# Performance work log

Measured on AMD Instinct MI355X. Metric: run time of the kernel, lower is better.

The kernel has to match this reference:

```python
import jax, jax.numpy as jnp
import numpy as np

D = 1024
H = 16
B = 4
S = 2048
NEG = -1000000000.0


def setup_inputs() -> dict:
    key = jax.random.key(0)
    ks = jax.random.split(key, 12)
    s = 0.02
    inp = {
        "Q": jax.random.normal(ks[0], (B, S, D), jnp.float32),
        "K": jax.random.normal(ks[1], (B, S, D), jnp.float32),
        "V": jax.random.normal(ks[2], (B, S, D), jnp.float32),
        # causal mask, broadcastable to [B, H, S, S]
        "mask": jnp.broadcast_to(jnp.tril(jnp.ones((S, S), bool)), (B, 1, S, S)),
        "Wq": jax.random.normal(ks[3], (D, D), jnp.float32) * s,
        "bq": jnp.zeros((D,), jnp.float32),
        "Wk": jax.random.normal(ks[4], (D, D), jnp.float32) * s,
        "bk": jnp.zeros((D,), jnp.float32),
        "Wv": jax.random.normal(ks[5], (D, D), jnp.float32) * s,
        "bv": jnp.zeros((D,), jnp.float32),
        "Wo": jax.random.normal(ks[6], (D, D), jnp.float32) * s,
        "bo": jnp.zeros((D,), jnp.float32),
    }
    return inp


def reference(Q, K, V, mask, Wq, bq, Wk, bk, Wv, bv, Wo, bo):
    d = D // H  # head dim
    def split(x):  # [B,S,D] -> [B,H,S,d]
        Bx, Sx, _ = x.shape
        return x.reshape(Bx, Sx, H, d).transpose(0, 2, 1, 3)

    q = split(Q @ Wq + bq)
    k = split(K @ Wk + bk)
    v = split(V @ Wv + bv)

    scores = jnp.einsum("bhsd,bhtd->bhst", q, k) / jnp.sqrt(jnp.float32(d))
    scores = jnp.where(mask, scores, NEG)
    attn = jax.nn.softmax(scores, axis=-1)
    out = jnp.einsum("bhst,bhtd->bhsd", attn, v)  # [B,H,S,d]
    out = out.transpose(0, 2, 1, 3).reshape(Q.shape[0], Q.shape[1], D)
    return out @ Wo + bo
```

## Files before the change

kernel.cpp:

```cpp
#include <hip/hip_runtime.h>
#include <hip/hip_bf16.h>
#include <type_traits>

#define DEV __device__ __forceinline__

typedef short bf16x8 __attribute__((ext_vector_type(8)));
typedef float f32x4 __attribute__((ext_vector_type(4)));
typedef float f32x16 __attribute__((ext_vector_type(16)));
typedef unsigned u32x4 __attribute__((ext_vector_type(4)));

static DEV unsigned short f2bf(float f) {
  unsigned u = __builtin_bit_cast(unsigned, f);
  u += 0x7FFFu + ((u >> 16) & 1u);
  return (unsigned short)(u >> 16);
}

static DEV unsigned cvtpk(float lo, float hi) {
  unsigned d;
  asm("v_cvt_pk_bf16_f32 %0, %1, %2" : "=v"(d) : "v"(lo), "v"(hi));
  return d;
}

static DEV void pl32(unsigned& x, unsigned& y) {
  asm("v_permlane32_swap_b32 %0, %1" : "+v"(x), "+v"(y));
}

static DEV float vmax3(float a, float b, float c) {
  float d;
  asm("v_max3_f32 %0, %1, %2, %3" : "=v"(d) : "v"(a), "v"(b), "v"(c));
  return d;
}

static DEV void gl_lds16(const unsigned short* g, unsigned short* l) {
  __builtin_amdgcn_global_load_lds(
      (const __attribute__((address_space(1))) unsigned*)g,
      (__attribute__((address_space(3))) unsigned*)l, 16, 0, 0);
}

#define QSCALE 0.18033688f

__global__ __launch_bounds__(256) void wtrans4(const float* __restrict__ W0,
                                               const float* __restrict__ W1,
                                               const float* __restrict__ W2,
                                               const float* __restrict__ W3,
                                               unsigned short* __restrict__ T0,
                                               unsigned short* __restrict__ T1,
                                               unsigned short* __restrict__ T2,
                                               unsigned short* __restrict__ T3) {
  const int z = blockIdx.z;
  const float* W = z == 0 ? W0 : z == 1 ? W1 : z == 2 ? W2 : W3;
  unsigned short* Wt = z == 0 ? T0 : z == 1 ? T1 : z == 2 ? T2 : T3;
  const float wsc = (z == 0) ? QSCALE : 1.0f;
  __shared__ __align__(16) unsigned short T[64][72];
  const int tid = threadIdx.x;
  const int k0 = blockIdx.x * 64, n0 = blockIdx.y * 64;
  const int r = tid >> 4, c4 = (tid & 15) * 4;
  for (int j = 0; j < 4; ++j) {
    int row = j * 16 + r;
    float4 v = *(const float4*)&W[(size_t)(k0 + row) * 1024 + n0 + c4];
    ushort4 w;
    w.x = f2bf(v.x * wsc); w.y = f2bf(v.y * wsc);
    w.z = f2bf(v.z * wsc); w.w = f2bf(v.w * wsc);
    *(ushort4*)&T[row][c4] = w;
  }
  __syncthreads();
  for (int j = 0; j < 4; ++j) {
    int n = j * 16 + r;
    ushort4 w;
    w.x = T[c4 + 0][n]; w.y = T[c4 + 1][n]; w.z = T[c4 + 2][n]; w.w = T[c4 + 3][n];
    *(ushort4*)&Wt[(size_t)(n0 + n) * 1024 + k0 + c4] = w;
  }
}

__global__ __launch_bounds__(256) void xcvt3(const float* __restrict__ S0,
                                             const float* __restrict__ S1,
                                             const float* __restrict__ S2,
                                             unsigned short* __restrict__ D0,
                                             unsigned short* __restrict__ D1,
                                             unsigned short* __restrict__ D2) {
  const int z = blockIdx.z;
  const float* S = z == 0 ? S0 : z == 1 ? S1 : S2;
  unsigned short* D = z == 0 ? D0 : z == 1 ? D1 : D2;
  const size_t stride = (size_t)gridDim.x * 256 * 8;
  for (size_t i = ((size_t)blockIdx.x * 256 + threadIdx.x) * 8; i < 8u * 1024 * 1024;
       i += stride) {
    float4 a = *(const float4*)&S[i];
    float4 b = *(const float4*)&S[i + 4];
    uint4 w;
    w.x = cvtpk(a.x, a.y);
    w.y = cvtpk(a.z, a.w);
    w.z = cvtpk(b.x, b.y);
    w.w = cvtpk(b.z, b.w);
    *(uint4*)&D[i] = w;
  }
}

template <typename OutT>
DEV void gemm_lds_body(const unsigned short* __restrict__ X,
                       const unsigned short* __restrict__ Wt,
                       const float* __restrict__ bias, OutT* __restrict__ Y,
                       float bsc) {
  __shared__ __align__(16) unsigned short As[128 * 64];
  __shared__ __align__(16) unsigned short Bs[128 * 64];
  const int tid = threadIdx.x, lane = tid & 63, wid = tid >> 6;
  const int m0 = blockIdx.x * 128, n0 = blockIdx.y * 128;
  const int wm = (wid >> 1) * 64, wn = (wid & 1) * 64;
  f32x4 acc[4][4] = {};

  const int srow = wid * 32 + (lane >> 3);
  const int scol = (((lane & 7) ^ ((lane >> 3) & 7))) * 8;
  const unsigned short* gA = &X[(size_t)(m0 + srow) * 1024 + scol];
  const unsigned short* gB = &Wt[(size_t)(n0 + srow) * 1024 + scol];
  unsigned short* lA = &As[wid * 32 * 64];
  unsigned short* lB = &Bs[wid * 32 * 64];

  for (int k0 = 0; k0 < 1024; k0 += 64) {
    __syncthreads();
#pragma unroll
    for (int j = 0; j < 4; ++j) {
      gl_lds16(gA + (size_t)j * 8 * 1024 + k0, lA + j * 8 * 64);
      gl_lds16(gB + (size_t)j * 8 * 1024 + k0, lB + j * 8 * 64);
    }
    __syncthreads();
#pragma unroll
    for (int kk = 0; kk < 2; ++kk) {
      const int kb = ((kk * 4 + (lane >> 4)) ^ (lane & 7)) * 8;
      bf16x8 af[4], bfr[4];
#pragma unroll
      for (int i = 0; i < 4; ++i)
        af[i] = *(const bf16x8*)&As[(wm + i * 16 + (lane & 15)) * 64 + kb];
#pragma unroll
      for (int i = 0; i < 4; ++i)
        bfr[i] = *(const bf16x8*)&Bs[(wn + i * 16 + (lane & 15)) * 64 + kb];
      __builtin_amdgcn_s_setprio(1);
#pragma unroll
      for (int mi = 0; mi < 4; ++mi)
#pragma unroll
        for (int ni = 0; ni < 4; ++ni)
          acc[mi][ni] =
              __builtin_amdgcn_mfma_f32_16x16x32_bf16(af[mi], bfr[ni], acc[mi][ni], 0, 0, 0);
      __builtin_amdgcn_s_setprio(0);
    }
  }
  for (int ni = 0; ni < 4; ++ni) {
    const int col = n0 + wn + ni * 16 + (lane & 15);
    const float bv = bias[col] * bsc;
    for (int mi = 0; mi < 4; ++mi) {
      const int row = m0 + wm + mi * 16 + (lane >> 4) * 4;
      for (int r = 0; r < 4; ++r) {
        float v = acc[mi][ni][r] + bv;
        if constexpr (std::is_same_v<OutT, float>)
          Y[(size_t)(row + r) * 1024 + col] = v;
        else
          Y[(size_t)(row + r) * 1024 + col] = f2bf(v);
      }
    }
  }
}

__global__ __launch_bounds__(256) void gemm_qkv3(
    const unsigned short* __restrict__ X0, const unsigned short* __restrict__ X1,
    const unsigned short* __restrict__ X2, const unsigned short* __restrict__ W0,
    const unsigned short* __restrict__ W1, const unsigned short* __restrict__ W2,
    const float* __restrict__ b0, const float* __restrict__ b1,
    const float* __restrict__ b2, unsigned short* __restrict__ Y0,
    unsigned short* __restrict__ Y1, unsigned short* __restrict__ Y2) {
  const int z = blockIdx.z;
  const unsigned short* X = z == 0 ? X0 : z == 1 ? X1 : X2;
  const unsigned short* Wt = z == 0 ? W0 : z == 1 ? W1 : W2;
  const float* bias = z == 0 ? b0 : z == 1 ? b1 : b2;
  unsigned short* Y = z == 0 ? Y0 : z == 1 ? Y1 : Y2;
  gemm_lds_body<unsigned short>(X, Wt, bias, Y, z == 0 ? QSCALE : 1.0f);
}

__global__ __launch_bounds__(256) void gemm_out(const unsigned short* __restrict__ X,
                                                const unsigned short* __restrict__ Wt,
                                                const float* __restrict__ bias,
                                                float* __restrict__ Y) {
  gemm_lds_body<float>(X, Wt, bias, Y, 1.0f);
}

__global__ __launch_bounds__(256) void vtrans(const unsigned short* __restrict__ vbf,
                                              unsigned short* __restrict__ vt) {
  __shared__ __align__(16) unsigned short T[64][72];
  const int tid = threadIdx.x;
  const int s0 = blockIdx.x * 64;
  const int bh = blockIdx.y, b = bh >> 4, h = bh & 15;
  const int col0 = h * 64;
  const int rr = tid >> 3, c8 = (tid & 7) * 8;
  for (int p = 0; p < 2; ++p) {
    const int row = rr + 32 * p;
    *(uint4*)&T[row][c8] =
        *(const uint4*)&vbf[((size_t)b * 2048 + s0 + row) * 1024 + col0 + c8];
  }
  __syncthreads();
  const int dv = tid & 63, ss = (tid >> 6) * 16;
  union { uint4 v[2]; unsigned short s[16]; } o;
#pragma unroll
  for (int i = 0; i < 16; ++i) o.s[i] = T[ss + i][dv];
  *(uint4*)&vt[((size_t)bh * 64 + dv) * 2048 + s0 + ss] = o.v[0];
  *(uint4*)&vt[((size_t)bh * 64 + dv) * 2048 + s0 + ss + 8] = o.v[1];
}

__global__ __launch_bounds__(256) void attn_fwd(const unsigned short* __restrict__ Qb,
                                                const unsigned short* __restrict__ Kb,
                                                const unsigned short* __restrict__ Vt,
                                                unsigned short* __restrict__ Ob) {
  constexpr int KP = 72;
  __shared__ __align__(16) unsigned short SM[4 * 64 * KP];
  const int tid = threadIdx.x, lane = tid & 63, wid = tid >> 6;
  const int l31 = lane & 31, hi = lane >> 5;
  const int id = blockIdx.x;
  const int xcd = id & 7, idx = id >> 3;
  const int bh = xcd + 8 * (idx & 7);
  const int pairidx = idx >> 3;
  const int b = bh >> 4, h = bh & 15;
  const size_t rowbase = (size_t)b * 2048;
  const int col0 = h * 64;
  const unsigned short* Vrow = Vt + (size_t)bh * 64 * 2048;
  const int rr = tid >> 3, c8 = (tid & 7) * 8;

  for (int half = 0; half < 2; ++half) {
    const int qb = half == 0 ? pairidx : 15 - pairidx;
    const int q0 = (15 - qb) * 128;
    const int qmin = q0 + wid * 32;
    const int myq = qmin + l31;

    bf16x8 qf[4];
#pragma unroll
    for (int c = 0; c < 4; ++c)
      qf[c] = *(const bf16x8*)&Qb[(rowbase + myq) * 1024 + col0 + c * 16 + hi * 8];

    f32x16 o[2];
    o[0] = 0.f; o[1] = 0.f;
    float mrow = -1.0e30f, lrow = 0.f;

    const int ntiles = q0 / 64 + 2;
    uint4 kr0, kr1, vr0, vr1;
#define LOADT(KV0)                                                              \
  do {                                                                          \
    const int _k = (KV0);                                                       \
    kr0 = *(const uint4*)&Kb[(rowbase + _k + rr) * 1024 + col0 + c8];           \
    kr1 = *(const uint4*)&Kb[(rowbase + _k + rr + 32) * 1024 + col0 + c8];      \
    vr0 = *(const uint4*)&Vrow[(size_t)rr * 2048 + _k + c8];                    \
    vr1 = *(const uint4*)&Vrow[(size_t)(rr + 32) * 2048 + _k + c8];             \
  } while (0)

    LOADT(0);
    {
      unsigned short* Ks = SM;
      unsigned short* Vs = SM + 64 * KP;
      *(uint4*)&Ks[rr * KP + c8] = kr0;
      *(uint4*)&Ks[(rr + 32) * KP + c8] = kr1;
      *(uint4*)&Vs[rr * KP + c8] = vr0;
      *(uint4*)&Vs[(rr + 32) * KP + c8] = vr1;
      LOADT(64);
      __syncthreads();
    }

    for (int t = 0; t < ntiles; ++t) {
      const int kv0 = t * 64;
      const int p = t & 1;
      if (kv0 <= qmin + 31) {
        const unsigned short* Ks = SM + p * 128 * KP;
        const unsigned short* Vs = Ks + 64 * KP;

        f32x16 s2[2];
        s2[0] = 0.f; s2[1] = 0.f;
        __builtin_amdgcn_s_setprio(1);
#pragma unroll
        for (int m = 0; m < 2; ++m)
#pragma unroll
          for (int c = 0; c < 4; ++c) {
            bf16x8 kf = *(const bf16x8*)&Ks[(m * 32 + l31) * KP + c * 16 + hi * 8];
            s2[m] = __builtin_amdgcn_mfma_f32_32x32x16_bf16(kf, qf[c], s2[m], 0, 0, 0);
          }
        __builtin_amdgcn_s_setprio(0);

        if (kv0 + 63 > qmin) {
          const int thr = l31 + (qmin - kv0);
#pragma unroll
          for (int m = 0; m < 2; ++m)
#pragma unroll
            for (int r = 0; r < 16; ++r) {
              const int kvl = m * 32 + (r & 3) + 8 * (r >> 2) + 4 * hi;
              if (kvl > thr) s2[m][r] = -1.0e30f;
            }
        }

        float tmax = fmaxf(s2[0][0], s2[0][1]);
#pragma unroll
        for (int m = 0; m < 2; ++m)
#pragma unroll
          for (int r = m == 0 ? 2 : 0; r < 16; r += 2)
            tmax = vmax3(tmax, s2[m][r], s2[m][r + 1]);
        tmax = fmaxf(tmax, __shfl_xor(tmax, 32));
        if (__any(tmax > mrow + 11.5f)) {
          const float mnew = fmaxf(mrow, tmax);
          const float al = __builtin_amdgcn_exp2f(mrow - mnew);
          mrow = mnew;
          lrow *= al;
          o[0] *= al;
          o[1] *= al;
        }
        float rs0 = 0.f, rs1 = 0.f;
#pragma unroll
        for (int m = 0; m < 2; ++m)
#pragma unroll
          for (int r = 0; r < 16; ++r) {
            const float pz = __builtin_amdgcn_exp2f(s2[m][r] - mrow);
            s2[m][r] = pz;
            if (r & 1) rs1 += pz; else rs0 += pz;
          }
        float rs = rs0 + rs1;
        rs += __shfl_xor(rs, 32);
        lrow += rs;

        bf16x8 pf[4];
#pragma unroll
        for (int m = 0; m < 2; ++m) {
          unsigned a0 = cvtpk(s2[m][0], s2[m][1]), a1 = cvtpk(s2[m][2], s2[m][3]);
          unsigned b0 = cvtpk(s2[m][4], s2[m][5]), b1 = cvtpk(s2[m][6], s2[m][7]);
          pl32(a0, b0);
          pl32(a1, b1);
          pf[2 * m] = __builtin_bit_cast(bf16x8, (u32x4){a0, a1, b0, b1});
          unsigned c0 = cvtpk(s2[m][8], s2[m][9]), c1 = cvtpk(s2[m][10], s2[m][11]);
          unsigned d0 = cvtpk(s2[m][12], s2[m][13]), d1 = cvtpk(s2[m][14], s2[m][15]);
          pl32(c0, d0);
          pl32(c1, d1);
          pf[2 * m + 1] = __builtin_bit_cast(bf16x8, (u32x4){c0, c1, d0, d1});
        }

        __builtin_amdgcn_s_setprio(1);
#pragma unroll
        for (int nt = 0; nt < 2; ++nt)
#pragma unroll
          for (int cc = 0; cc < 4; ++cc) {
            bf16x8 vf = *(const bf16x8*)&Vs[(nt * 32 + l31) * KP + cc * 16 + hi * 8];
            o[nt] = __builtin_amdgcn_mfma_f32_32x32x16_bf16(vf, pf[cc], o[nt], 0, 0, 0);
          }
        __builtin_amdgcn_s_setprio(0);
      }
      if (t + 1 < ntiles) {
        unsigned short* Ks = SM + (p ^ 1) * 128 * KP;
        unsigned short* Vs = Ks + 64 * KP;
        *(uint4*)&Ks[rr * KP + c8] = kr0;
        *(uint4*)&Ks[(rr + 32) * KP + c8] = kr1;
        *(uint4*)&Vs[rr * KP + c8] = vr0;
        *(uint4*)&Vs[(rr + 32) * KP + c8] = vr1;
        if (t + 2 < ntiles) LOADT(kv0 + 128);
      }
      __syncthreads();
    }
#undef LOADT

    unsigned short* Os = SM + wid * 32 * KP;
    const float inv = 1.0f / lrow;
#pragma unroll
    for (int nt = 0; nt < 2; ++nt)
#pragma unroll
      for (int rq = 0; rq < 4; ++rq)
#pragma unroll
        for (int j = 0; j < 2; ++j) {
          const int r = rq * 4 + 2 * j;
          const unsigned pk = cvtpk(o[nt][r] * inv, o[nt][r + 1] * inv);
          *(unsigned*)&Os[l31 * KP + nt * 32 + 8 * rq + 4 * hi + 2 * j] = pk;
        }
    __syncthreads();
#pragma unroll
    for (int i = 0; i < 4; ++i) {
      const int qq = (lane >> 3) + i * 8;
      const int dvc = (lane & 7) * 8;
      uint4 val = *(const uint4*)&Os[qq * KP + dvc];
      *(uint4*)&Ob[(rowbase + qmin + qq) * 1024 + col0 + dvc] = val;
    }
    __syncthreads();
  }
}

extern "C" void kernel_launch(void* const* d_in, const int* in_sizes, int n_in,
                              void* d_out, int out_size, void* d_ws, size_t ws_size,
                              hipStream_t stream) {
  const float* Q  = (const float*)d_in[0];
  const float* K  = (const float*)d_in[1];
  const float* V  = (const float*)d_in[2];
  const float* Wq = (const float*)d_in[4];
  const float* bq = (const float*)d_in[5];
  const float* Wk = (const float*)d_in[6];
  const float* bk = (const float*)d_in[7];
  const float* Wv = (const float*)d_in[8];
  const float* bv = (const float*)d_in[9];
  const float* Wo = (const float*)d_in[10];
  const float* bo = (const float*)d_in[11];
  float* out = (float*)d_out;

  const size_t MB = 1024 * 1024;
  char* ws = (char*)d_ws;
  unsigned short* qb  = (unsigned short*)(ws + 0 * MB);
  unsigned short* kb  = (unsigned short*)(ws + 16 * MB);
  unsigned short* vbf = (unsigned short*)(ws + 32 * MB);
  unsigned short* vt  = (unsigned short*)(ws + 48 * MB);
  unsigned short* wtq = (unsigned short*)(ws + 64 * MB);
  unsigned short* wtk = (unsigned short*)(ws + 66 * MB);
  unsigned short* wtv = (unsigned short*)(ws + 68 * MB);
  unsigned short* wto = (unsigned short*)(ws + 70 * MB);
  unsigned short* ob  = vbf;

  wtrans4<<<dim3(16, 16, 4), 256, 0, stream>>>(Wq, Wk, Wv, Wo, wtq, wtk, wtv, wto);

  if (ws_size >= 120 * MB) {
    unsigned short* qx = (unsigned short*)(ws + 72 * MB);
    unsigned short* kx = (unsigned short*)(ws + 88 * MB);
    unsigned short* vx = (unsigned short*)(ws + 104 * MB);
    xcvt3<<<dim3(2048, 1, 3), 256, 0, stream>>>(Q, K, V, qx, kx, vx);
    gemm_qkv3<<<dim3(64, 8, 3), 256, 0, stream>>>(qx, kx, vx, wtq, wtk, wtv,
                                                  bq, bk, bv, qb, kb, vbf);
  } else {
    unsigned short* xb = vt;
    const float* Xs[3] = {Q, K, V};
    const unsigned short* Ws[3] = {wtq, wtk, wtv};
    const float* Bs[3] = {bq, bk, bv};
    unsigned short* Ys[3] = {qb, kb, vbf};
    for (int t = 0; t < 3; ++t) {
      xcvt3<<<dim3(2048, 1, 1), 256, 0, stream>>>(Xs[t], Xs[t], Xs[t], xb, xb, xb);
      gemm_qkv3<<<dim3(64, 8, 1), 256, 0, stream>>>(xb, xb, xb, Ws[t], Ws[t], Ws[t],
                                                    Bs[t], Bs[t], Bs[t],
                                                    Ys[t], Ys[t], Ys[t]);
    }
  }

  vtrans<<<dim3(32, 64), 256, 0, stream>>>(vbf, vt);

  attn_fwd<<<512, 256, 0, stream>>>(qb, kb, vt, ob);

  gemm_out<<<dim3(64, 8), 256, 0, stream>>>(ob, wto, bo, out);
}
```

Baseline: 201.1 us.

## Process both causal query blocks concurrently in 512-thread attention blocks sharing K/V tiles

The attention kernel previously looped over two query blocks (a short and a long causal range) sequentially in a 256-thread block. It now launches 512 threads, with waves 0-3 handling one query block and waves 4-7 the other, both consuming the same K/V tiles staged in shared memory. This halves the per-block K/V global traffic and LDS staging for the shared prefix and doubles waves available to hide latency. Waves of the shorter block sit idle at barriers while the longer block finishes its extra tiles, and larger blocks may reduce occupancy.

```diff
diff --git a/kernel.cpp b/kernel.cpp
--- a/kernel.cpp
+++ b/kernel.cpp
@@ -202,7 +202,7 @@
   *(uint4*)&vt[((size_t)bh * 64 + dv) * 2048 + s0 + ss + 8] = o.v[1];
 }
 
-__global__ __launch_bounds__(256) void attn_fwd(const unsigned short* __restrict__ Qb,
+__global__ __launch_bounds__(512) void attn_fwd(const unsigned short* __restrict__ Qb,
                                                 const unsigned short* __restrict__ Kb,
                                                 const unsigned short* __restrict__ Vt,
                                                 unsigned short* __restrict__ Ob) {
@@ -220,161 +220,153 @@
   const unsigned short* Vrow = Vt + (size_t)bh * 64 * 2048;
   const int rr = tid >> 3, c8 = (tid & 7) * 8;
 
-  for (int half = 0; half < 2; ++half) {
-    const int qb = half == 0 ? pairidx : 15 - pairidx;
-    const int q0 = (15 - qb) * 128;
-    const int qmin = q0 + wid * 32;
-    const int myq = qmin + l31;
-
-    bf16x8 qf[4];
-#pragma unroll
-    for (int c = 0; c < 4; ++c)
-      qf[c] = *(const bf16x8*)&Qb[(rowbase + myq) * 1024 + col0 + c * 16 + hi * 8];
-
-    f32x16 o[2];
-    o[0] = 0.f; o[1] = 0.f;
-    float mrow = -1.0e30f, lrow = 0.f;
-
-    const int ntiles = q0 / 64 + 2;
-    uint4 kr0, kr1, vr0, vr1;
-#define LOADT(KV0)                                                              \
-  do {                                                                          \
-    const int _k = (KV0);                                                       \
-    kr0 = *(const uint4*)&Kb[(rowbase + _k + rr) * 1024 + col0 + c8];           \
-    kr1 = *(const uint4*)&Kb[(rowbase + _k + rr + 32) * 1024 + col0 + c8];      \
-    vr0 = *(const uint4*)&Vrow[(size_t)rr * 2048 + _k + c8];                    \
-    vr1 = *(const uint4*)&Vrow[(size_t)(rr + 32) * 2048 + _k + c8];             \
+  const int half = wid >> 2, w4 = wid & 3;
+  const int qb = half == 0 ? pairidx : 15 - pairidx;
+  const int q0 = (15 - qb) * 128;
+  const int qmin = q0 + w4 * 32;
+  const int myq = qmin + l31;
+  const int NT = (15 - pairidx) * 2 + 2;
+
+  bf16x8 qf[4];
+#pragma unroll
+  for (int c = 0; c < 4; ++c)
+    qf[c] = *(const bf16x8*)&Qb[(rowbase + myq) * 1024 + col0 + c * 16 + hi * 8];
+
+  f32x16 o[2];
+  o[0] = 0.f; o[1] = 0.f;
+  float mrow = -1.0e30f, lrow = 0.f;
+
+  uint4 kr, vr;
+#define LOADT(KV0)                                                           \
+  do {                                                                       \
+    const int _k = (KV0);                                                    \
+    kr = *(const uint4*)&Kb[(rowbase + _k + rr) * 1024 + col0 + c8];         \
+    vr = *(const uint4*)&Vrow[(size_t)rr * 2048 + _k + c8];                  \
   } while (0)
 
-    LOADT(0);
-    {
-      unsigned short* Ks = SM;
-      unsigned short* Vs = SM + 64 * KP;
-      *(uint4*)&Ks[rr * KP + c8] = kr0;
-      *(uint4*)&Ks[(rr + 32) * KP + c8] = kr1;
-      *(uint4*)&Vs[rr * KP + c8] = vr0;
-      *(uint4*)&Vs[(rr + 32) * KP + c8] = vr1;
-      LOADT(64);
-      __syncthreads();
-    }
-
-    for (int t = 0; t < ntiles; ++t) {
-      const int kv0 = t * 64;
-      const int p = t & 1;
-      if (kv0 <= qmin + 31) {
-        const unsigned short* Ks = SM + p * 128 * KP;
-        const unsigned short* Vs = Ks + 64 * KP;
-
-        f32x16 s2[2];
-        s2[0] = 0.f; s2[1] = 0.f;
-        __builtin_amdgcn_s_setprio(1);
+  LOADT(0);
+  {
+    unsigned short* Ks = SM;
+    unsigned short* Vs = SM + 64 * KP;
+    *(uint4*)&Ks[rr * KP + c8] = kr;
+    *(uint4*)&Vs[rr * KP + c8] = vr;
+    if (NT > 1) LOADT(64);
+    __syncthreads();
+  }
+
+  for (int t = 0; t < NT; ++t) {
+    const int kv0 = t * 64;
+    const int p = t & 1;
+    if (kv0 <= qmin + 31) {
+      const unsigned short* Ks = SM + p * 128 * KP;
+      const unsigned short* Vs = Ks + 64 * KP;
+
+      f32x16 s2[2];
+      s2[0] = 0.f; s2[1] = 0.f;
+      __builtin_amdgcn_s_setprio(1);
+#pragma unroll
+      for (int m = 0; m < 2; ++m)
+#pragma unroll
+        for (int c = 0; c < 4; ++c) {
+          bf16x8 kf = *(const bf16x8*)&Ks[(m * 32 + l31) * KP + c * 16 + hi * 8];
+          s2[m] = __builtin_amdgcn_mfma_f32_32x32x16_bf16(kf, qf[c], s2[m], 0, 0, 0);
+        }
+      __builtin_amdgcn_s_setprio(0);
+
+      if (kv0 + 63 > qmin) {
+        const int thr = l31 + (qmin - kv0);
 #pragma unroll
         for (int m = 0; m < 2; ++m)
 #pragma unroll
-          for (int c = 0; c < 4; ++c) {
-            bf16x8 kf = *(const bf16x8*)&Ks[(m * 32 + l31) * KP + c * 16 + hi * 8];
-            s2[m] = __builtin_amdgcn_mfma_f32_32x32x16_bf16(kf, qf[c], s2[m], 0, 0, 0);
+          for (int r = 0; r < 16; ++r) {
+            const int kvl = m * 32 + (r & 3) + 8 * (r >> 2) + 4 * hi;
+            if (kvl > thr) s2[m][r] = -1.0e30f;
           }
-        __builtin_amdgcn_s_setprio(0);
-
-        if (kv0 + 63 > qmin) {
-          const int thr = l31 + (qmin - kv0);
-#pragma unroll
-          for (int m = 0; m < 2; ++m)
-#pragma unroll
-            for (int r = 0; r < 16; ++r) {
-              const int kvl = m * 32 + (r & 3) + 8 * (r >> 2) + 4 * hi;
-              if (kvl > thr) s2[m][r] = -1.0e30f;
-            }
+      }
+
+      float tmax = fmaxf(s2[0][0], s2[0][1]);
+#pragma unroll
+      for (int m = 0; m < 2; ++m)
+#pragma unroll
+        for (int r = m == 0 ? 2 : 0; r < 16; r += 2)
+          tmax = vmax3(tmax, s2[m][r], s2[m][r + 1]);
+      tmax = fmaxf(tmax, __shfl_xor(tmax, 32));
+      if (__any(tmax > mrow + 11.5f)) {
+        const float mnew = fmaxf(mrow, tmax);
+        const float al = __builtin_amdgcn_exp2f(mrow - mnew);
+        mrow = mnew;
+        lrow *= al;
+        o[0] *= al;
+        o[1] *= al;
+      }
+      float rs0 = 0.f, rs1 = 0.f;
+#pragma unroll
+      for (int m = 0; m < 2; ++m)
+#pragma unroll
+        for (int r = 0; r < 16; ++r) {
+          const float pz = __builtin_amdgcn_exp2f(s2[m][r] - mrow);
+          s2[m][r] = pz;
+          if (r & 1) rs1 += pz; else rs0 += pz;
         }
-
-        float tmax = fmaxf(s2[0][0], s2[0][1]);
-#pragma unroll
-        for (int m = 0; m < 2; ++m)
-#pragma unroll
-          for (int r = m == 0 ? 2 : 0; r < 16; r += 2)
-            tmax = vmax3(tmax, s2[m][r], s2[m][r + 1]);
-        tmax = fmaxf(tmax, __shfl_xor(tmax, 32));
-        if (__any(tmax > mrow + 11.5f)) {
-          const float mnew = fmaxf(mrow, tmax);
-          const float al = __builtin_amdgcn_exp2f(mrow - mnew);
-          mrow = mnew;
-          lrow *= al;
-          o[0] *= al;
-          o[1] *= al;
+      float rs = rs0 + rs1;
+      rs += __shfl_xor(rs, 32);
+      lrow += rs;
+
+      bf16x8 pf[4];
+#pragma unroll
+      for (int m = 0; m < 2; ++m) {
+        unsigned a0 = cvtpk(s2[m][0], s2[m][1]), a1 = cvtpk(s2[m][2], s2[m][3]);
+        unsigned b0 = cvtpk(s2[m][4], s2[m][5]), b1 = cvtpk(s2[m][6], s2[m][7]);
+        pl32(a0, b0);
+        pl32(a1, b1);
+        pf[2 * m] = __builtin_bit_cast(bf16x8, (u32x4){a0, a1, b0, b1});
+        unsigned c0 = cvtpk(s2[m][8], s2[m][9]), c1 = cvtpk(s2[m][10], s2[m][11]);
+        unsigned d0 = cvtpk(s2[m][12], s2[m][13]), d1 = cvtpk(s2[m][14], s2[m][15]);
+        pl32(c0, d0);
+        pl32(c1, d1);
+        pf[2 * m + 1] = __builtin_bit_cast(bf16x8, (u32x4){c0, c1, d0, d1});
+      }
+
+      __builtin_amdgcn_s_setprio(1);
+#pragma unroll
+      for (int nt = 0; nt < 2; ++nt)
+#pragma unroll
+        for (int cc = 0; cc < 4; ++cc) {
+          bf16x8 vf = *(const bf16x8*)&Vs[(nt * 32 + l31) * KP + cc * 16 + hi * 8];
+          o[nt] = __builtin_amdgcn_mfma_f32_32x32x16_bf16(vf, pf[cc], o[nt], 0, 0, 0);
         }
-        float rs0 = 0.f, rs1 = 0.f;
-#pragma unroll
-        for (int m = 0; m < 2; ++m)
-#pragma unroll
-          for (int r = 0; r < 16; ++r) {
-            const float pz = __builtin_amdgcn_exp2f(s2[m][r] - mrow);
-            s2[m][r] = pz;
-            if (r & 1) rs1 += pz; else rs0 += pz;
-          }
-        float rs = rs0 + rs1;
-        rs += __shfl_xor(rs, 32);
-        lrow += rs;
-
-        bf16x8 pf[4];
-#pragma unroll
-        for (int m = 0; m < 2; ++m) {
-          unsigned a0 = cvtpk(s2[m][0], s2[m][1]), a1 = cvtpk(s2[m][2], s2[m][3]);
-          unsigned b0 = cvtpk(s2[m][4], s2[m][5]), b1 = cvtpk(s2[m][6], s2[m][7]);
-          pl32(a0, b0);
-          pl32(a1, b1);
-          pf[2 * m] = __builtin_bit_cast(bf16x8, (u32x4){a0, a1, b0, b1});
-          unsigned c0 = cvtpk(s2[m][8], s2[m][9]), c1 = cvtpk(s2[m][10], s2[m][11]);
-          unsigned d0 = cvtpk(s2[m][12], s2[m][13]), d1 = cvtpk(s2[m][14], s2[m][15]);
-          pl32(c0, d0);
-          pl32(c1, d1);
-          pf[2 * m + 1] = __builtin_bit_cast(bf16x8, (u32x4){c0, c1, d0, d1});
-        }
-
-        __builtin_amdgcn_s_setprio(1);
-#pragma unroll
-        for (int nt = 0; nt < 2; ++nt)
-#pragma unroll
-          for (int cc = 0; cc < 4; ++cc) {
-            bf16x8 vf = *(const bf16x8*)&Vs[(nt * 32 + l31) * KP + cc * 16 + hi * 8];
-            o[nt] = __builtin_amdgcn_mfma_f32_32x32x16_bf16(vf, pf[cc], o[nt], 0, 0, 0);
-          }
-        __builtin_amdgcn_s_setprio(0);
+      __builtin_amdgcn_s_setprio(0);
+    }
+    if (t + 1 < NT) {
+      unsigned short* Ks = SM + (p ^ 1) * 128 * KP;
+      unsigned short* Vs = Ks + 64 * KP;
+      *(uint4*)&Ks[rr * KP + c8] = kr;
+      *(uint4*)&Vs[rr * KP + c8] = vr;
+      if (t + 2 < NT) LOADT(kv0 + 128);
+    }
+    __syncthreads();
+  }
+#undef LOADT
+
+  unsigned short* Os = SM + wid * 32 * KP;
+  const float inv = 1.0f / lrow;
+#pragma unroll
+  for (int nt = 0; nt < 2; ++nt)
+#pragma unroll
+    for (int rq = 0; rq < 4; ++rq)
+#pragma unroll
+      for (int j = 0; j < 2; ++j) {
+        const int r = rq * 4 + 2 * j;
+        const unsigned pk = cvtpk(o[nt][r] * inv, o[nt][r + 1] * inv);
+        *(unsigned*)&Os[l31 * KP + nt * 32 + 8 * rq + 4 * hi + 2 * j] = pk;
       }
-      if (t + 1 < ntiles) {
-        unsigned short* Ks = SM + (p ^ 1) * 128 * KP;
-        unsigned short* Vs = Ks + 64 * KP;
-        *(uint4*)&Ks[rr * KP + c8] = kr0;
-        *(uint4*)&Ks[(rr + 32) * KP + c8] = kr1;
-        *(uint4*)&Vs[rr * KP + c8] = vr0;
-        *(uint4*)&Vs[(rr + 32) * KP + c8] = vr1;
-        if (t + 2 < ntiles) LOADT(kv0 + 128);
-      }
-      __syncthreads();
-    }
-#undef LOADT
-
-    unsigned short* Os = SM + wid * 32 * KP;
-    const float inv = 1.0f / lrow;
-#pragma unroll
-    for (int nt = 0; nt < 2; ++nt)
-#pragma unroll
-      for (int rq = 0; rq < 4; ++rq)
-#pragma unroll
-        for (int j = 0; j < 2; ++j) {
-          const int r = rq * 4 + 2 * j;
-          const unsigned pk = cvtpk(o[nt][r] * inv, o[nt][r + 1] * inv);
-          *(unsigned*)&Os[l31 * KP + nt * 32 + 8 * rq + 4 * hi + 2 * j] = pk;
-        }
-    __syncthreads();
-#pragma unroll
-    for (int i = 0; i < 4; ++i) {
-      const int qq = (lane >> 3) + i * 8;
-      const int dvc = (lane & 7) * 8;
-      uint4 val = *(const uint4*)&Os[qq * KP + dvc];
-      *(uint4*)&Ob[(rowbase + qmin + qq) * 1024 + col0 + dvc] = val;
-    }
-    __syncthreads();
+  __syncthreads();
+#pragma unroll
+  for (int i = 0; i < 4; ++i) {
+    const int qq = (lane >> 3) + i * 8;
+    const int dvc = (lane & 7) * 8;
+    uint4 val = *(const uint4*)&Os[qq * KP + dvc];
+    *(uint4*)&Ob[(rowbase + qmin + qq) * 1024 + col0 + dvc] = val;
   }
 }
 
@@ -431,7 +423,7 @@
 
   vtrans<<<dim3(32, 64), 256, 0, stream>>>(vbf, vt);
 
-  attn_fwd<<<512, 256, 0, stream>>>(qb, kb, vt, ob);
+  attn_fwd<<<512, 512, 0, stream>>>(qb, kb, vt, ob);
 
   gemm_out<<<dim3(64, 8), 256, 0, stream>>>(ob, wto, bo, out);
 }
```

Measured after the change: 199.4 us. No clear change (-0.8%).

## Split paired causal q-blocks into separate workgroups and compute row sums via MFMA

Applied to the files above, without the earlier changes.

Each workgroup previously handled two query blocks (a short and a long one) to balance the causal workload. Now there is one query block per workgroup and the grid is twice as large, which adds parallelism at the cost of relying on the hardware scheduler for load balance. The softmax row-sum reduction, previously a VALU sum plus a cross-lane shuffle, is replaced by an extra MFMA against a ones vector, so the sums are taken over the bf16-rounded probabilities. This moves work from the vector ALU to the matrix units but adds four MFMAs per tile.

```diff
diff --git a/kernel.cpp b/kernel.cpp
--- a/kernel.cpp
+++ b/kernel.cpp
@@ -213,30 +213,30 @@
   const int id = blockIdx.x;
   const int xcd = id & 7, idx = id >> 3;
   const int bh = xcd + 8 * (idx & 7);
-  const int pairidx = idx >> 3;
+  const int qb = idx >> 3;
+  const int q0 = (15 - qb) * 128;
   const int b = bh >> 4, h = bh & 15;
   const size_t rowbase = (size_t)b * 2048;
   const int col0 = h * 64;
+  const int qmin = q0 + wid * 32;
+  const int myq = qmin + l31;
   const unsigned short* Vrow = Vt + (size_t)bh * 64 * 2048;
   const int rr = tid >> 3, c8 = (tid & 7) * 8;
 
-  for (int half = 0; half < 2; ++half) {
-    const int qb = half == 0 ? pairidx : 15 - pairidx;
-    const int q0 = (15 - qb) * 128;
-    const int qmin = q0 + wid * 32;
-    const int myq = qmin + l31;
-
-    bf16x8 qf[4];
-#pragma unroll
-    for (int c = 0; c < 4; ++c)
-      qf[c] = *(const bf16x8*)&Qb[(rowbase + myq) * 1024 + col0 + c * 16 + hi * 8];
-
-    f32x16 o[2];
-    o[0] = 0.f; o[1] = 0.f;
-    float mrow = -1.0e30f, lrow = 0.f;
-
-    const int ntiles = q0 / 64 + 2;
-    uint4 kr0, kr1, vr0, vr1;
+  bf16x8 qf[4];
+#pragma unroll
+  for (int c = 0; c < 4; ++c)
+    qf[c] = *(const bf16x8*)&Qb[(rowbase + myq) * 1024 + col0 + c * 16 + hi * 8];
+
+  const bf16x8 onesv =
+      __builtin_bit_cast(bf16x8, (u32x4){0x3F803F80u, 0x3F803F80u, 0x3F803F80u, 0x3F803F80u});
+
+  f32x16 o[2], rsa;
+  o[0] = 0.f; o[1] = 0.f; rsa = 0.f;
+  float mrow = -1.0e30f;
+
+  const int NT = q0 / 64 + 2;
+  uint4 kr0, kr1, vr0, vr1;
 #define LOADT(KV0)                                                              \
   do {                                                                          \
     const int _k = (KV0);                                                       \
@@ -246,135 +246,129 @@
     vr1 = *(const uint4*)&Vrow[(size_t)(rr + 32) * 2048 + _k + c8];             \
   } while (0)
 
-    LOADT(0);
-    {
-      unsigned short* Ks = SM;
-      unsigned short* Vs = SM + 64 * KP;
+  LOADT(0);
+  {
+    unsigned short* Ks = SM;
+    unsigned short* Vs = SM + 64 * KP;
+    *(uint4*)&Ks[rr * KP + c8] = kr0;
+    *(uint4*)&Ks[(rr + 32) * KP + c8] = kr1;
+    *(uint4*)&Vs[rr * KP + c8] = vr0;
+    *(uint4*)&Vs[(rr + 32) * KP + c8] = vr1;
+    LOADT(64);
+    __syncthreads();
+  }
+
+  for (int t = 0; t < NT; ++t) {
+    const int kv0 = t * 64;
+    const int p = t & 1;
+    if (kv0 <= qmin + 31) {
+      const unsigned short* Ks = SM + p * 128 * KP;
+      const unsigned short* Vs = Ks + 64 * KP;
+
+      f32x16 s2[2];
+      s2[0] = 0.f; s2[1] = 0.f;
+      __builtin_amdgcn_s_setprio(1);
+#pragma unroll
+      for (int m = 0; m < 2; ++m)
+#pragma unroll
+        for (int c = 0; c < 4; ++c) {
+          bf16x8 kf = *(const bf16x8*)&Ks[(m * 32 + l31) * KP + c * 16 + hi * 8];
+          s2[m] = __builtin_amdgcn_mfma_f32_32x32x16_bf16(kf, qf[c], s2[m], 0, 0, 0);
+        }
+      __builtin_amdgcn_s_setprio(0);
+
+      if (kv0 + 63 > qmin) {
+        const int thr = l31 + (qmin - kv0);
+#pragma unroll
+        for (int m = 0; m < 2; ++m)
+#pragma unroll
+          for (int r = 0; r < 16; ++r) {
+            const int kvl = m * 32 + (r & 3) + 8 * (r >> 2) + 4 * hi;
+            if (kvl > thr) s2[m][r] = -1.0e30f;
+          }
+      }
+
+      float tmax = fmaxf(s2[0][0], s2[0][1]);
+#pragma unroll
+      for (int m = 0; m < 2; ++m)
+#pragma unroll
+        for (int r = m == 0 ? 2 : 0; r < 16; r += 2)
+          tmax = vmax3(tmax, s2[m][r], s2[m][r + 1]);
+      tmax = fmaxf(tmax, __shfl_xor(tmax, 32));
+      if (__any(tmax > mrow + 11.5f)) {
+        const float mnew = fmaxf(mrow, tmax);
+        const float al = __builtin_amdgcn_exp2f(mrow - mnew);
+        mrow = mnew;
+        o[0] *= al;
+        o[1] *= al;
+        rsa[0] *= al;
+      }
+#pragma unroll
+      for (int m = 0; m < 2; ++m)
+#pragma unroll
+        for (int r = 0; r < 16; ++r)
+          s2[m][r] = __builtin_amdgcn_exp2f(s2[m][r] - mrow);
+
+      bf16x8 pf[4];
+#pragma unroll
+      for (int m = 0; m < 2; ++m) {
+        unsigned a0 = cvtpk(s2[m][0], s2[m][1]), a1 = cvtpk(s2[m][2], s2[m][3]);
+        unsigned b0 = cvtpk(s2[m][4], s2[m][5]), b1 = cvtpk(s2[m][6], s2[m][7]);
+        pl32(a0, b0);
+        pl32(a1, b1);
+        pf[2 * m] = __builtin_bit_cast(bf16x8, (u32x4){a0, a1, b0, b1});
+        unsigned c0 = cvtpk(s2[m][8], s2[m][9]), c1 = cvtpk(s2[m][10], s2[m][11]);
+        unsigned d0 = cvtpk(s2[m][12], s2[m][13]), d1 = cvtpk(s2[m][14], s2[m][15]);
+        pl32(c0, d0);
+        pl32(c1, d1);
+        pf[2 * m + 1] = __builtin_bit_cast(bf16x8, (u32x4){c0, c1, d0, d1});
+      }
+
+      __builtin_amdgcn_s_setprio(1);
+#pragma unroll
+      for (int nt = 0; nt < 2; ++nt)
+#pragma unroll
+        for (int cc = 0; cc < 4; ++cc) {
+          bf16x8 vf = *(const bf16x8*)&Vs[(nt * 32 + l31) * KP + cc * 16 + hi * 8];
+          o[nt] = __builtin_amdgcn_mfma_f32_32x32x16_bf16(vf, pf[cc], o[nt], 0, 0, 0);
+        }
+#pragma unroll
+      for (int cc = 0; cc < 4; ++cc)
+        rsa = __builtin_amdgcn_mfma_f32_32x32x16_bf16(onesv, pf[cc], rsa, 0, 0, 0);
+      __builtin_amdgcn_s_setprio(0);
+    }
+    if (t + 1 < NT) {
+      unsigned short* Ks = SM + (p ^ 1) * 128 * KP;
+      unsigned short* Vs = Ks + 64 * KP;
       *(uint4*)&Ks[rr * KP + c8] = kr0;
       *(uint4*)&Ks[(rr + 32) * KP + c8] = kr1;
       *(uint4*)&Vs[rr * KP + c8] = vr0;
       *(uint4*)&Vs[(rr + 32) * KP + c8] = vr1;
-      LOADT(64);
-      __syncthreads();
-    }
-
-    for (int t = 0; t < ntiles; ++t) {
-      const int kv0 = t * 64;
-      const int p = t & 1;
-      if (kv0 <= qmin + 31) {
-        const unsigned short* Ks = SM + p * 128 * KP;
-        const unsigned short* Vs = Ks + 64 * KP;
-
-        f32x16 s2[2];
-        s2[0] = 0.f; s2[1] = 0.f;
-        __builtin_amdgcn_s_setprio(1);
-#pragma unroll
-        for (int m = 0; m < 2; ++m)
-#pragma unroll
-          for (int c = 0; c < 4; ++c) {
-            bf16x8 kf = *(const bf16x8*)&Ks[(m * 32 + l31) * KP + c * 16 + hi * 8];
-            s2[m] = __builtin_amdgcn_mfma_f32_32x32x16_bf16(kf, qf[c], s2[m], 0, 0, 0);
-          }
-        __builtin_amdgcn_s_setprio(0);
-
-        if (kv0 + 63 > qmin) {
-          const int thr = l31 + (qmin - kv0);
-#pragma unroll
-          for (int m = 0; m < 2; ++m)
-#pragma unroll
-            for (int r = 0; r < 16; ++r) {
-              const int kvl = m * 32 + (r & 3) + 8 * (r >> 2) + 4 * hi;
-              if (kvl > thr) s2[m][r] = -1.0e30f;
-            }
-        }
-
-        float tmax = fmaxf(s2[0][0], s2[0][1]);
-#pragma unroll
-        for (int m = 0; m < 2; ++m)
-#pragma unroll
-          for (int r = m == 0 ? 2 : 0; r < 16; r += 2)
-            tmax = vmax3(tmax, s2[m][r], s2[m][r + 1]);
-        tmax = fmaxf(tmax, __shfl_xor(tmax, 32));
-        if (__any(tmax > mrow + 11.5f)) {
-          const float mnew = fmaxf(mrow, tmax);
-          const float al = __builtin_amdgcn_exp2f(mrow - mnew);
-          mrow = mnew;
-          lrow *= al;
-          o[0] *= al;
-          o[1] *= al;
-        }
-        float rs0 = 0.f, rs1 = 0.f;
-#pragma unroll
-        for (int m = 0; m < 2; ++m)
-#pragma unroll
-          for (int r = 0; r < 16; ++r) {
-            const float pz = __builtin_amdgcn_exp2f(s2[m][r] - mrow);
-            s2[m][r] = pz;
-            if (r & 1) rs1 += pz; else rs0 += pz;
-          }
-        float rs = rs0 + rs1;
-        rs += __shfl_xor(rs, 32);
-        lrow += rs;
-
-        bf16x8 pf[4];
-#pragma unroll
-        for (int m = 0; m < 2; ++m) {
-          unsigned a0 = cvtpk(s2[m][0], s2[m][1]), a1 = cvtpk(s2[m][2], s2[m][3]);
-          unsigned b0 = cvtpk(s2[m][4], s2[m][5]), b1 = cvtpk(s2[m][6], s2[m][7]);
-          pl32(a0, b0);
-          pl32(a1, b1);
-          pf[2 * m] = __builtin_bit_cast(bf16x8, (u32x4){a0, a1, b0, b1});
-          unsigned c0 = cvtpk(s2[m][8], s2[m][9]), c1 = cvtpk(s2[m][10], s2[m][11]);
-          unsigned d0 = cvtpk(s2[m][12], s2[m][13]), d1 = cvtpk(s2[m][14], s2[m][15]);
-          pl32(c0, d0);
-          pl32(c1, d1);
-          pf[2 * m + 1] = __builtin_bit_cast(bf16x8, (u32x4){c0, c1, d0, d1});
-        }
-
-        __builtin_amdgcn_s_setprio(1);
-#pragma unroll
-        for (int nt = 0; nt < 2; ++nt)
-#pragma unroll
-          for (int cc = 0; cc < 4; ++cc) {
-            bf16x8 vf = *(const bf16x8*)&Vs[(nt * 32 + l31) * KP + cc * 16 + hi * 8];
-            o[nt] = __builtin_amdgcn_mfma_f32_32x32x16_bf16(vf, pf[cc], o[nt], 0, 0, 0);
-          }
-        __builtin_amdgcn_s_setprio(0);
+      if (t + 2 < NT) LOADT(kv0 + 128);
+    }
+    __syncthreads();
+  }
+#undef LOADT
+
+  unsigned short* Os = SM + wid * 32 * KP;
+  const float inv = 1.0f / rsa[0];
+#pragma unroll
+  for (int nt = 0; nt < 2; ++nt)
+#pragma unroll
+    for (int rq = 0; rq < 4; ++rq)
+#pragma unroll
+      for (int j = 0; j < 2; ++j) {
+        const int r = rq * 4 + 2 * j;
+        const unsigned pk = cvtpk(o[nt][r] * inv, o[nt][r + 1] * inv);
+        *(unsigned*)&Os[l31 * KP + nt * 32 + 8 * rq + 4 * hi + 2 * j] = pk;
       }
-      if (t + 1 < ntiles) {
-        unsigned short* Ks = SM + (p ^ 1) * 128 * KP;
-        unsigned short* Vs = Ks + 64 * KP;
-        *(uint4*)&Ks[rr * KP + c8] = kr0;
-        *(uint4*)&Ks[(rr + 32) * KP + c8] = kr1;
-        *(uint4*)&Vs[rr * KP + c8] = vr0;
-        *(uint4*)&Vs[(rr + 32) * KP + c8] = vr1;
-        if (t + 2 < ntiles) LOADT(kv0 + 128);
-      }
-      __syncthreads();
-    }
-#undef LOADT
-
-    unsigned short* Os = SM + wid * 32 * KP;
-    const float inv = 1.0f / lrow;
-#pragma unroll
-    for (int nt = 0; nt < 2; ++nt)
-#pragma unroll
-      for (int rq = 0; rq < 4; ++rq)
-#pragma unroll
-        for (int j = 0; j < 2; ++j) {
-          const int r = rq * 4 + 2 * j;
-          const unsigned pk = cvtpk(o[nt][r] * inv, o[nt][r + 1] * inv);
-          *(unsigned*)&Os[l31 * KP + nt * 32 + 8 * rq + 4 * hi + 2 * j] = pk;
-        }
-    __syncthreads();
-#pragma unroll
-    for (int i = 0; i < 4; ++i) {
-      const int qq = (lane >> 3) + i * 8;
-      const int dvc = (lane & 7) * 8;
-      uint4 val = *(const uint4*)&Os[qq * KP + dvc];
-      *(uint4*)&Ob[(rowbase + qmin + qq) * 1024 + col0 + dvc] = val;
-    }
-    __syncthreads();
+  __syncthreads();
+#pragma unroll
+  for (int i = 0; i < 4; ++i) {
+    const int qq = (lane >> 3) + i * 8;
+    const int dvc = (lane & 7) * 8;
+    uint4 val = *(const uint4*)&Os[qq * KP + dvc];
+    *(uint4*)&Ob[(rowbase + qmin + qq) * 1024 + col0 + dvc] = val;
   }
 }
 
@@ -431,7 +425,7 @@
 
   vtrans<<<dim3(32, 64), 256, 0, stream>>>(vbf, vt);
 
-  attn_fwd<<<512, 256, 0, stream>>>(qb, kb, vt, ob);
+  attn_fwd<<<1024, 256, 0, stream>>>(qb, kb, vt, ob);
 
   gemm_out<<<dim3(64, 8), 256, 0, stream>>>(ob, wto, bo, out);
 }
```

Result: no change. 200.4 us (-0.3%).
